# Kernel optimization log

Measured on AMD Instinct MI355X. Metric: run time of the kernel, lower is better.

The kernel has to match this reference:

```python
import jax, jax.numpy as jnp
import numpy as np

WS, SHIFT, NH, DIM = 8, 4, 4, 128
HD = DIM // NH
B, H, W = 16, 128, 128
N = WS * WS
LOG100 = float(np.log(100.0))


def _rel_tables():
    r = np.arange(-(WS - 1), WS, dtype=np.float32)
    tab = np.stack(np.meshgrid(r, r, indexing='ij'), axis=-1) / (WS - 1) * 8.0
    tab = np.sign(tab) * np.log2(np.abs(tab) + 1.0) / np.log2(8.0)
    coords = np.stack(np.meshgrid(np.arange(WS), np.arange(WS), indexing='ij')).reshape(2, -1)
    rel = (coords[:, :, None] - coords[:, None, :]).transpose(1, 2, 0).copy()
    rel[:, :, 0] += WS - 1
    rel[:, :, 1] += WS - 1
    rel[:, :, 0] *= 2 * WS - 1
    return jnp.asarray(tab.reshape(-1, 2)), jnp.asarray(rel.sum(-1))

REL_TABLE, REL_INDEX = _rel_tables()  # ((2WS-1)^2, 2), (N, N)


def _attn_mask():
    img = np.zeros((H, W), np.float32)
    cnt = 0
    for hs in (slice(0, -WS), slice(-WS, -SHIFT), slice(-SHIFT, None)):
        for ws in (slice(0, -WS), slice(-WS, -SHIFT), slice(-SHIFT, None)):
            img[hs, ws] = cnt
            cnt += 1
    mw = img.reshape(H // WS, WS, W // WS, WS).transpose(0, 2, 1, 3).reshape(-1, N)
    d = mw[:, None, :] - mw[:, :, None]
    return jnp.asarray(np.where(d != 0, -100.0, 0.0).astype(np.float32))

ATTN_MASK = _attn_mask()  # (nW, N, N)


def _ln(x, w, b, eps=1e-5):
    mu = x.mean(-1, keepdims=True)
    var = ((x - mu) ** 2).mean(-1, keepdims=True)
    return (x - mu) * jax.lax.rsqrt(var + eps) * w + b


def setup_inputs() -> dict:
    key = jax.random.key(0)
    ks = jax.random.split(key, 8)
    s = 0.02
    return {
        'x': jax.random.normal(ks[0], (B, DIM, H, W), jnp.float32),
        'norm1_w': jnp.ones((DIM,), jnp.float32),
        'norm1_b': jnp.zeros((DIM,), jnp.float32),
        'qkv_w': jax.random.normal(ks[1], (3 * DIM, DIM), jnp.float32) * s,
        'q_bias': jnp.zeros((DIM,), jnp.float32),
        'v_bias': jnp.zeros((DIM,), jnp.float32),
        'logit_scale': jnp.full((NH, 1, 1), float(np.log(10.0)), jnp.float32),
        'cpb_w1': jax.random.normal(ks[2], (512, 2), jnp.float32) * s,
        'cpb_b1': jnp.zeros((512,), jnp.float32),
        'cpb_w2': jax.random.normal(ks[3], (NH, 512), jnp.float32) * s,
        'proj_w': jax.random.normal(ks[4], (DIM, DIM), jnp.float32) * s,
        'proj_b': jnp.zeros((DIM,), jnp.float32),
        'norm2_w': jnp.ones((DIM,), jnp.float32),
        'norm2_b': jnp.zeros((DIM,), jnp.float32),
        'fc1_w': jax.random.normal(ks[5], (4 * DIM, DIM), jnp.float32) * s,
        'fc1_b': jnp.zeros((4 * DIM,), jnp.float32),
        'fc2_w': jax.random.normal(ks[6], (DIM, 4 * DIM), jnp.float32) * s,
        'fc2_b': jnp.zeros((DIM,), jnp.float32),
    }


def reference(x, norm1_w, norm1_b, qkv_w, q_bias, v_bias, logit_scale,
              cpb_w1, cpb_b1, cpb_w2, proj_w, proj_b,
              norm2_w, norm2_b, fc1_w, fc1_b, fc2_w, fc2_b):
    xb = jnp.transpose(x, (0, 2, 3, 1))                 # (B,H,W,C)
    shortcut = xb.reshape(B, H * W, DIM)
    shifted = jnp.roll(xb, (-SHIFT, -SHIFT), axis=(1, 2))
    # window partition -> (B*nW, N, C)
    xw = shifted.reshape(B, H // WS, WS, W // WS, WS, DIM)
    xw = xw.transpose(0, 1, 3, 2, 4, 5).reshape(-1, N, DIM)
    B_ = xw.shape[0]
    qkv_bias = jnp.concatenate([q_bias, jnp.zeros_like(v_bias), v_bias])
    qkv = xw @ qkv_w.T + qkv_bias
    qkv = qkv.reshape(B_, N, 3, NH, HD).transpose(2, 0, 3, 1, 4)
    q, k, v = qkv[0], qkv[1], qkv[2]                    # (B_,NH,N,HD)
    qn = q / jnp.maximum(jnp.linalg.norm(q, axis=-1, keepdims=True), 1e-12)
    kn = k / jnp.maximum(jnp.linalg.norm(k, axis=-1, keepdims=True), 1e-12)
    attn = jnp.einsum('bhnd,bhmd->bhnm', qn, kn)
    attn = attn * jnp.exp(jnp.minimum(logit_scale, LOG100))
    # continuous relative position bias: tiny MLP over log-spaced coords + gather
    tab = jax.nn.relu(REL_TABLE @ cpb_w1.T + cpb_b1) @ cpb_w2.T    # ((2WS-1)^2, NH)
    bias = tab[REL_INDEX.reshape(-1)].reshape(N, N, NH).transpose(2, 0, 1)
    attn = attn + (16.0 * jax.nn.sigmoid(bias))[None]
    nW = ATTN_MASK.shape[0]
    attn = attn.reshape(B_ // nW, nW, NH, N, N) + ATTN_MASK[None, :, None]
    attn = jax.nn.softmax(attn.reshape(B_, NH, N, N), axis=-1)
    out = jnp.einsum('bhnm,bhmd->bhnd', attn, v).transpose(0, 2, 1, 3).reshape(B_, N, DIM)
    out = out @ proj_w.T + proj_b
    # window reverse + reverse cyclic shift
    out = out.reshape(B, H // WS, W // WS, WS, WS, DIM).transpose(0, 1, 3, 2, 4, 5).reshape(B, H, W, DIM)
    out = jnp.roll(out, (SHIFT, SHIFT), axis=(1, 2)).reshape(B, H * W, DIM)
    x1 = shortcut + _ln(out, norm1_w, norm1_b)          # Swin-v2 post-norm residual
    hdn = jax.nn.silu(x1 @ fc1_w.T + fc1_b) @ fc2_w.T + fc2_b
    x2 = x1 + _ln(hdn, norm2_w, norm2_b)
    return x2.reshape(B, H, W, DIM).transpose(0, 3, 1, 2)
```

## Files before the change

### kernel.cpp

```cpp
#include <hip/hip_runtime.h>
#include <cstdint>
#include <cstddef>

typedef __bf16 bf16;
typedef __bf16 bf16x4 __attribute__((ext_vector_type(4)));
typedef __bf16 bf16x8 __attribute__((ext_vector_type(8)));
typedef float f32x4 __attribute__((ext_vector_type(4)));

#define MFMA16(a, b, c) __builtin_amdgcn_mfma_f32_16x16x32_bf16((a), (b), (c), 0, 0, 0)

__device__ __forceinline__ float bf2f(bf16 v) { return (float)v; }

__device__ __forceinline__ void pack4(float a0, float a1, float a2, float a3, bf16* dst) {
    bf16x4 v; v[0] = (bf16)a0; v[1] = (bf16)a1; v[2] = (bf16)a2; v[3] = (bf16)a3;
    *(bf16x4*)dst = v;
}

#define OFF_SCALES 65536
#define OFF_FLAG   65552
#define OFF_QKVB   65600
#define OFF_PROJB  67136
#define OFF_N1W    67648
#define OFF_N1B    68160
#define OFF_FC1B   68672
#define OFF_FC2B   70720
#define OFF_N2W    71232
#define OFF_N2B    71744
#define OFF_QKVW   73728
#define OFF_PROJW  172032
#define OFF_FC1W   204800
#define OFF_FC2W   335872

template<int DT>
__device__ __forceinline__ void g_ld4(const void* base, size_t idx, float* o) {
    if constexpr (DT == 0) {
        uint2 d = *(const uint2*)((const bf16*)base + idx);
        const bf16* p = (const bf16*)&d;
        o[0] = bf2f(p[0]); o[1] = bf2f(p[1]); o[2] = bf2f(p[2]); o[3] = bf2f(p[3]);
    } else {
        float4 d = *(const float4*)((const float*)base + idx);
        o[0] = d.x; o[1] = d.y; o[2] = d.z; o[3] = d.w;
    }
}

__global__ void k_init(const void* __restrict__ cpb_w1, const void* __restrict__ cpb_b1,
                       const void* __restrict__ cpb_w2, const void* __restrict__ logit_scale,
                       const void* __restrict__ qkv_w, const void* __restrict__ proj_w,
                       const void* __restrict__ fc1w, const void* __restrict__ fc2w,
                       const void* __restrict__ q_bias, const void* __restrict__ v_bias,
                       const void* __restrict__ proj_b, const void* __restrict__ n1w, const void* __restrict__ n1b,
                       const void* __restrict__ fc1b, const void* __restrict__ fc2b,
                       const void* __restrict__ n2w, const void* __restrict__ n2b,
                       char* __restrict__ ws)
{
    const int t = threadIdx.x;
    __shared__ int s_cnt;
    if (t == 0) s_cnt = 0;
    __syncthreads();
    {
        const unsigned short* u = (const unsigned short*)qkv_w;
        int c = 0;
        for (int i = t; i < 1024; i += 256) {
            const int e = (u[i] >> 7) & 0xFF;
            if (e >= 0x90 || (e != 0 && e <= 0x60)) ++c;
        }
        atomicAdd(&s_cnt, c);
    }
    __syncthreads();
    const int isf = (s_cnt > 64) ? 1 : 0;

    if (blockIdx.x == 0) {
        float* biasAll = (float*)ws;
        float* scales  = (float*)(ws + OFF_SCALES);
        int*   flag    = (int*)(ws + OFF_FLAG);
        if (t == 0) *flag = isf;
        __shared__ float w1s[1024];
        __shared__ float b1s[512];
        __shared__ float w2s[2048];
        __shared__ float tabv[225][4];
        if (isf) {
            const float* w1 = (const float*)cpb_w1;
            const float* b1 = (const float*)cpb_b1;
            const float* w2 = (const float*)cpb_w2;
            for (int i = t; i < 1024; i += 256) w1s[i] = w1[i];
            for (int i = t; i < 512;  i += 256) b1s[i] = b1[i];
            for (int i = t; i < 2048; i += 256) w2s[i] = w2[i];
            if (t < 4) scales[t] = expf(fminf(((const float*)logit_scale)[t], 4.6051701859880914f));
        } else {
            const bf16* w1 = (const bf16*)cpb_w1;
            const bf16* b1 = (const bf16*)cpb_b1;
            const bf16* w2 = (const bf16*)cpb_w2;
            for (int i = t; i < 1024; i += 256) w1s[i] = bf2f(w1[i]);
            for (int i = t; i < 512;  i += 256) b1s[i] = bf2f(b1[i]);
            for (int i = t; i < 2048; i += 256) w2s[i] = bf2f(w2[i]);
            if (t < 4) scales[t] = expf(fminf(bf2f(((const bf16*)logit_scale)[t]), 4.6051701859880914f));
        }
        __syncthreads();
        if (t < 225) {
            const int i = t / 15, j = t % 15;
            auto relf = [](int tt) -> float {
                float tf = (float)tt * (8.0f / 7.0f);
                float a = log2f(fabsf(tf) + 1.0f) * (1.0f / 3.0f);
                return tt < 0 ? -a : a;
            };
            const float x0 = relf(i - 7), x1 = relf(j - 7);
            float a0 = 0.f, a1 = 0.f, a2 = 0.f, a3 = 0.f;
            for (int jj = 0; jj < 512; ++jj) {
                float hv = w1s[jj*2] * x0 + w1s[jj*2+1] * x1 + b1s[jj];
                hv = fmaxf(hv, 0.0f);
                a0 += w2s[jj]        * hv;
                a1 += w2s[512 + jj]  * hv;
                a2 += w2s[1024 + jj] * hv;
                a3 += w2s[1536 + jj] * hv;
            }
            tabv[t][0] = a0; tabv[t][1] = a1; tabv[t][2] = a2; tabv[t][3] = a3;
        }
        __syncthreads();
        for (int idx = t; idx < 4*64*64; idx += 256) {
            const int h = idx >> 12, rem = idx & 4095, i = rem >> 6, j = rem & 63;
            const int di = (i >> 3) - (j >> 3) + 7;
            const int dj = (i & 7) - (j & 7) + 7;
            const float bv = tabv[di*15 + dj][h];
            biasAll[idx] = 16.0f / (1.0f + expf(-bv));
        }
    } else {
        const int g  = (blockIdx.x - 1) * 256 + t;
        const int gs = 96 * 256;
        bf16* qw = (bf16*)(ws + OFF_QKVW);
        bf16* pw = (bf16*)(ws + OFF_PROJW);
        bf16* f1 = (bf16*)(ws + OFF_FC1W);
        bf16* f2 = (bf16*)(ws + OFF_FC2W);
        if (isf) {
            const float* a = (const float*)qkv_w;  for (int i = g; i < 49152; i += gs) qw[i] = (bf16)a[i];
            const float* b = (const float*)proj_w; for (int i = g; i < 16384; i += gs) pw[i] = (bf16)b[i];
            const float* c = (const float*)fc1w;   for (int i = g; i < 65536; i += gs) f1[i] = (bf16)c[i];
            const float* d = (const float*)fc2w;   for (int i = g; i < 65536; i += gs) f2[i] = (bf16)d[i];
        } else {
            const bf16* a = (const bf16*)qkv_w;  for (int i = g; i < 49152; i += gs) qw[i] = a[i];
            const bf16* b = (const bf16*)proj_w; for (int i = g; i < 16384; i += gs) pw[i] = b[i];
            const bf16* c = (const bf16*)fc1w;   for (int i = g; i < 65536; i += gs) f1[i] = c[i];
            const bf16* d = (const bf16*)fc2w;   for (int i = g; i < 65536; i += gs) f2[i] = d[i];
        }
        auto ldf = [&](const void* p, int i) -> float {
            return isf ? ((const float*)p)[i] : bf2f(((const bf16*)p)[i]);
        };
        float* qb  = (float*)(ws + OFF_QKVB);
        float* pb  = (float*)(ws + OFF_PROJB);
        float* w1  = (float*)(ws + OFF_N1W);
        float* b1  = (float*)(ws + OFF_N1B);
        float* f1b = (float*)(ws + OFF_FC1B);
        float* f2b = (float*)(ws + OFF_FC2B);
        float* w2  = (float*)(ws + OFF_N2W);
        float* b2  = (float*)(ws + OFF_N2B);
        for (int i = g; i < 384; i += gs)
            qb[i] = (i < 128) ? ldf(q_bias, i) : ((i < 256) ? 0.0f : ldf(v_bias, i - 256));
        for (int i = g; i < 512; i += gs) f1b[i] = ldf(fc1b, i);
        for (int i = g; i < 128; i += gs) {
            pb[i]  = ldf(proj_b, i); w1[i] = ldf(n1w, i); b1[i] = ldf(n1b, i);
            f2b[i] = ldf(fc2b, i);   w2[i] = ldf(n2w, i); b2[i] = ldf(n2b, i);
        }
    }
}

__global__ __launch_bounds__(256, 3) void k_fused(
    const void* __restrict__ x,
    const bf16* __restrict__ qkvw, const float* __restrict__ qkvb,
    const bf16* __restrict__ projw, const float* __restrict__ projb,
    const float* __restrict__ n1wf, const float* __restrict__ n1bf,
    const bf16* __restrict__ fc1w, const float* __restrict__ fc1bf,
    const bf16* __restrict__ fc2w, const float* __restrict__ fc2bf,
    const float* __restrict__ n2wf, const float* __restrict__ n2bf,
    const float* __restrict__ biasAll, const float* __restrict__ scales,
    const int* __restrict__ flag, void* __restrict__ out)
{
    const int isf = *flag;

    __shared__ __align__(16) char smem[52480];
    char* XK   = smem;
    bf16* x1s  = (bf16*)smem;
    char* R3   = smem + 32768;
    bf16* Xs   = (bf16*)R3;
    bf16* Os   = (bf16*)R3;
    bf16* hs   = (bf16*)R3;
    float* psum  = (float*)(smem + 50176);
    float* invks = psum;
    float* pvar  = (float*)(smem + 51200);
    int*   rid   = (int*)(smem + 52224);

    const int tid  = threadIdx.x;
    const int wv   = tid >> 6;
    const int lane = tid & 63;
    const int l15  = lane & 15;
    const int quad = lane >> 4;

    const int bid0 = blockIdx.x;
    const int bid  = ((bid0 & 7) << 9) | (bid0 >> 3);
    const int b   = bid >> 8;
    const int wh  = (bid >> 4) & 15;
    const int ww  = bid & 15;

    {
        const int c  = tid & 127;
        const int rb = tid >> 7;
        const int w0 = ww*8 + 4;
        const int w1 = (ww*8 + 8) & 127;
#pragma unroll
        for (int k = 0; k < 4; ++k) {
            const int r    = k*2 + rb;
            const int srch = (wh*8 + r + 4) & 127;
            const size_t rowbase = (((size_t)(b*128 + c))*128 + srch)*128;
            float va[4], vb[4];
            if (isf) { g_ld4<1>(x, rowbase + w0, va); g_ld4<1>(x, rowbase + w1, vb); }
            else     { g_ld4<0>(x, rowbase + w0, va); g_ld4<0>(x, rowbase + w1, vb); }
#pragma unroll
            for (int j = 0; j < 4; ++j) {
                Xs[(r*8 + j)*136 + c]     = (bf16)va[j];
                Xs[(r*8 + 4 + j)*136 + c] = (bf16)vb[j];
            }
        }
        if (tid < 64) {
            const int rr = tid >> 3, cc = tid & 7;
            const int hs_ = wh*8 + rr, wsc = ww*8 + cc;
            const int rh = (hs_ < 120) ? 0 : ((hs_ < 124) ? 1 : 2);
            const int rw = (wsc < 120) ? 0 : ((wsc < 124) ? 1 : 2);
            rid[tid] = rh*3 + rw;
        }
    }
    __syncthreads();

    float iq[4];
    {
        f32x4 acc[6][4];
#pragma unroll
        for (int t = 0; t < 6; ++t)
#pragma unroll
            for (int mt = 0; mt < 4; ++mt) acc[t][mt] = (f32x4){0.f, 0.f, 0.f, 0.f};
#pragma unroll
        for (int ks = 0; ks < 4; ++ks) {
            bf16x8 a[4];
#pragma unroll
            for (int mt = 0; mt < 4; ++mt)
                a[mt] = *(const bf16x8*)&Xs[(mt*16 + l15)*136 + ks*32 + quad*8];
#pragma unroll
            for (int t = 0; t < 6; ++t) {
                const int wrow = (t >> 1)*128 + wv*32 + (t & 1)*16 + l15;
                bf16x8 bw = *(const bf16x8*)&qkvw[(size_t)wrow*128 + ks*32 + quad*8];
                if (t < 4) {
#pragma unroll
                    for (int mt = 0; mt < 4; ++mt)
                        acc[t][mt] = MFMA16(bw, a[mt], acc[t][mt]);
                } else {
#pragma unroll
                    for (int mt = 0; mt < 4; ++mt)
                        acc[t][mt] = MFMA16(a[mt], bw, acc[t][mt]);
                }
            }
        }
        __syncthreads();

        float sq[4] = {0.f,0.f,0.f,0.f};
        float sk[4] = {0.f,0.f,0.f,0.f};
#pragma unroll
        for (int t = 0; t < 4; ++t) {
            const int colb = (t >> 1)*128 + wv*32 + (t & 1)*16 + quad*4;
            const float4 b4 = *(const float4*)&qkvb[colb];
#pragma unroll
            for (int mt = 0; mt < 4; ++mt) {
                const int row = mt*16 + l15;
                const float v0 = acc[t][mt][0] + b4.x;
                const float v1 = acc[t][mt][1] + b4.y;
                const float v2 = acc[t][mt][2] + b4.z;
                const float v3 = acc[t][mt][3] + b4.w;
                const float ss = v0*v0 + v1*v1 + v2*v2 + v3*v3;
                if (t < 2) sq[mt] += ss; else sk[mt] += ss;
                pack4(v0, v1, v2, v3,
                      (bf16*)(XK + row*512 + ((colb*2) ^ ((row & 7) << 4))));
            }
        }
#pragma unroll
        for (int t = 4; t < 6; ++t) {
            const int vrow = wv*32 + (t & 1)*16 + l15;
            const float bb = qkvb[256 + vrow];
            char* vbase = R3 + vrow*128;
            const int rx = (vrow & 7) << 4;
#pragma unroll
            for (int mt = 0; mt < 4; ++mt) {
                const int tokb = mt*16 + quad*4;
                pack4(acc[t][mt][0] + bb, acc[t][mt][1] + bb,
                      acc[t][mt][2] + bb, acc[t][mt][3] + bb,
                      (bf16*)(vbase + ((tokb*2) ^ rx)));
            }
        }
#pragma unroll
        for (int mt = 0; mt < 4; ++mt) {
            float s2 = sq[mt];
            s2 += __shfl_xor(s2, 16); s2 += __shfl_xor(s2, 32);
            iq[mt] = 1.0f / fmaxf(sqrtf(s2), 1e-12f);
            float k2 = sk[mt];
            k2 += __shfl_xor(k2, 16); k2 += __shfl_xor(k2, 32);
            if (quad == 0) invks[wv*64 + mt*16 + l15] = 1.0f / fmaxf(sqrtf(k2), 1e-12f);
        }
    }

    {
        const float scale = scales[wv];
        f32x4 s[4][4];
#pragma unroll
        for (int jt = 0; jt < 4; ++jt)
#pragma unroll
            for (int it = 0; it < 4; ++it) s[jt][it] = (f32x4){0.f, 0.f, 0.f, 0.f};
        bf16x8 aq[4];
#pragma unroll
        for (int it = 0; it < 4; ++it) {
            const int row = it*16 + l15;
            aq[it] = *(const bf16x8*)(XK + row*512 + (((wv*32 + quad*8)*2) ^ ((row & 7) << 4)));
        }
#pragma unroll
        for (int jt = 0; jt < 4; ++jt) {
            const int row = jt*16 + l15;
            bf16x8 bk = *(const bf16x8*)(XK + row*512 + (((128 + wv*32 + quad*8)*2) ^ ((row & 7) << 4)));
#pragma unroll
            for (int it = 0; it < 4; ++it)
                s[jt][it] = MFMA16(bk, aq[it], s[jt][it]);
        }
        __syncthreads();

        const float* bg = biasAll + wv*4096;
        const bool bnd = (wh == 15) || (ww == 15);
        float iqs[4]; int ri[4];
#pragma unroll
        for (int it = 0; it < 4; ++it) {
            iqs[it] = iq[it] * scale;
            ri[it]  = rid[it*16 + l15];
        }
        float4 ikj[4]; int4 rj4[4];
#pragma unroll
        for (int jt = 0; jt < 4; ++jt) {
            ikj[jt] = *(const float4*)&invks[wv*64 + jt*16 + quad*4];
            rj4[jt] = *(const int4*)&rid[jt*16 + quad*4];
        }
#pragma unroll
        for (int it = 0; it < 4; ++it) {
            const int i = it*16 + l15;
#pragma unroll
            for (int jt = 0; jt < 4; ++jt) {
                const float4 bb = *(const float4*)&bg[i*64 + jt*16 + quad*4];
#pragma unroll
                for (int r = 0; r < 4; ++r) {
                    float v = s[jt][it][r] * (iqs[it] * ((const float*)&ikj[jt])[r]) + ((const float*)&bb)[r];
                    if (bnd && (ri[it] != ((const int*)&rj4[jt])[r])) v -= 100.0f;
                    s[jt][it][r] = v;
                }
            }
            float m = s[0][it][0];
#pragma unroll
            for (int jt = 0; jt < 4; ++jt)
#pragma unroll
                for (int r = 0; r < 4; ++r) m = fmaxf(m, s[jt][it][r]);
            m = fmaxf(m, __shfl_xor(m, 16));
            m = fmaxf(m, __shfl_xor(m, 32));
            float sm = 0.f;
#pragma unroll
            for (int jt = 0; jt < 4; ++jt)
#pragma unroll
                for (int r = 0; r < 4; ++r) {
                    const float e = __expf(s[jt][it][r] - m);
                    s[jt][it][r] = e;
                    sm += e;
                }
            sm += __shfl_xor(sm, 16);
            sm += __shfl_xor(sm, 32);
            const float inv = 1.0f / sm;
#pragma unroll
            for (int jt = 0; jt < 4; ++jt)
                pack4(s[jt][it][0]*inv, s[jt][it][1]*inv, s[jt][it][2]*inv, s[jt][it][3]*inv,
                      (bf16*)(XK + wv*8192 + i*128 + ((jt*32 + quad*8) ^ ((i & 7) << 4))));
        }
    }

    {
        f32x4 o[2][4];
#pragma unroll
        for (int dt = 0; dt < 2; ++dt)
#pragma unroll
            for (int it = 0; it < 4; ++it) o[dt][it] = (f32x4){0.f, 0.f, 0.f, 0.f};
#pragma unroll
        for (int ks = 0; ks < 2; ++ks) {
            bf16x8 bp[4];
#pragma unroll
            for (int it = 0; it < 4; ++it) {
                const int row = it*16 + l15;
                bp[it] = *(const bf16x8*)(XK + wv*8192 + row*128 + ((ks*64 + quad*16) ^ ((row & 7) << 4)));
            }
#pragma unroll
            for (int dt = 0; dt < 2; ++dt) {
                const int vrow = wv*32 + dt*16 + l15;
                bf16x8 av = *(const bf16x8*)(R3 + vrow*128 + ((ks*64 + quad*16) ^ ((vrow & 7) << 4)));
#pragma unroll
                for (int it = 0; it < 4; ++it)
                    o[dt][it] = MFMA16(av, bp[it], o[dt][it]);
            }
        }
        __syncthreads();
#pragma unroll
        for (int dt = 0; dt < 2; ++dt)
#pragma unroll
            for (int it = 0; it < 4; ++it)
                pack4(o[dt][it][0], o[dt][it][1], o[dt][it][2], o[dt][it][3],
                      &Os[(it*16 + l15)*136 + wv*32 + dt*16 + quad*4]);
    }
    __syncthreads();

    {
        float res[2][4][4];
#pragma unroll
        for (int tt = 0; tt < 4; ++tt) {
            const int tok = tt*16 + l15;
            const int hh  = (wh*8 + (tok >> 3) + 4) & 127;
            const int wwp = (ww*8 + (tok & 7) + 4) & 127;
            const size_t tb = (size_t)b*2097152 + (size_t)hh*128 + wwp;
#pragma unroll
            for (int ct = 0; ct < 2; ++ct)
#pragma unroll
                for (int r = 0; r < 4; ++r) {
                    const int c = wv*32 + ct*16 + quad*4 + r;
                    float xv;
                    if (isf) xv = ((const float*)x)[tb + (size_t)c*16384];
                    else     xv = bf2f(((const bf16*)x)[tb + (size_t)c*16384]);
                    res[ct][tt][r] = bf2f((bf16)xv);
                }
        }
        f32x4 pa[2][4];
#pragma unroll
        for (int ct = 0; ct < 2; ++ct)
#pragma unroll
            for (int tt = 0; tt < 4; ++tt) pa[ct][tt] = (f32x4){0.f, 0.f, 0.f, 0.f};
#pragma unroll
        for (int ks = 0; ks < 4; ++ks) {
            bf16x8 bo[4];
#pragma unroll
            for (int tt = 0; tt < 4; ++tt)
                bo[tt] = *(const bf16x8*)&Os[(tt*16 + l15)*136 + ks*32 + quad*8];
#pragma unroll
            for (int ct = 0; ct < 2; ++ct) {
                bf16x8 aw = *(const bf16x8*)&projw[(size_t)(wv*32 + ct*16 + l15)*128 + ks*32 + quad*8];
#pragma unroll
                for (int tt = 0; tt < 4; ++tt)
                    pa[ct][tt] = MFMA16(aw, bo[tt], pa[ct][tt]);
            }
        }
        float4 pb4[2], wn4[2], bn4[2];
#pragma unroll
        for (int ct = 0; ct < 2; ++ct) {
            const int ob = wv*32 + ct*16 + quad*4;
            pb4[ct] = *(const float4*)&projb[ob];
            wn4[ct] = *(const float4*)&n1wf[ob];
            bn4[ct] = *(const float4*)&n1bf[ob];
        }
#pragma unroll
        for (int tt = 0; tt < 4; ++tt) {
            float sv = 0.f;
#pragma unroll
            for (int ct = 0; ct < 2; ++ct)
#pragma unroll
                for (int r = 0; r < 4; ++r) {
                    pa[ct][tt][r] += ((const float*)&pb4[ct])[r];
                    sv += pa[ct][tt][r];
                }
            sv += __shfl_xor(sv, 16);
            sv += __shfl_xor(sv, 32);
            if (quad == 0) psum[wv*64 + tt*16 + l15] = sv;
        }
        __syncthreads();
        float mu[4];
#pragma unroll
        for (int tt = 0; tt < 4; ++tt) {
            const int tok = tt*16 + l15;
            mu[tt] = (psum[tok] + psum[64+tok] + psum[128+tok] + psum[192+tok]) * (1.0f/128.0f);
            float sv = 0.f;
#pragma unroll
            for (int ct = 0; ct < 2; ++ct)
#pragma unroll
                for (int r = 0; r < 4; ++r) {
                    const float d = pa[ct][tt][r] - mu[tt];
                    sv += d*d;
                }
            sv += __shfl_xor(sv, 16);
            sv += __shfl_xor(sv, 32);
            if (quad == 0) pvar[wv*64 + tok] = sv;
        }
        __syncthreads();
#pragma unroll
        for (int tt = 0; tt < 4; ++tt) {
            const int tok = tt*16 + l15;
            const float var = (pvar[tok] + pvar[64+tok] + pvar[128+tok] + pvar[192+tok]) * (1.0f/128.0f);
            const float rstd = rsqrtf(var + 1e-5f);
#pragma unroll
            for (int ct = 0; ct < 2; ++ct) {
                const int ob = wv*32 + ct*16 + quad*4;
                float xv[4];
#pragma unroll
                for (int r = 0; r < 4; ++r)
                    xv[r] = res[ct][tt][r] + (pa[ct][tt][r] - mu[tt]) * rstd * ((const float*)&wn4[ct])[r]
                            + ((const float*)&bn4[ct])[r];
                pack4(xv[0], xv[1], xv[2], xv[3], &x1s[tok*136 + ob]);
            }
        }
    }
    __syncthreads();

    f32x4 ya[2][4];
#pragma unroll
    for (int ct = 0; ct < 2; ++ct)
#pragma unroll
        for (int tt = 0; tt < 4; ++tt) ya[ct][tt] = (f32x4){0.f, 0.f, 0.f, 0.f};

#pragma unroll
    for (int ch = 0; ch < 4; ++ch) {
        if (ch) __syncthreads();
        f32x4 ha[2][4];
#pragma unroll
        for (int ht = 0; ht < 2; ++ht)
#pragma unroll
            for (int tt = 0; tt < 4; ++tt) ha[ht][tt] = (f32x4){0.f, 0.f, 0.f, 0.f};
#pragma unroll
        for (int ks = 0; ks < 4; ++ks) {
            bf16x8 bx[4];
#pragma unroll
            for (int tt = 0; tt < 4; ++tt)
                bx[tt] = *(const bf16x8*)&x1s[(tt*16 + l15)*136 + ks*32 + quad*8];
#pragma unroll
            for (int ht = 0; ht < 2; ++ht) {
                bf16x8 aw = *(const bf16x8*)&fc1w[(size_t)(ch*128 + wv*32 + ht*16 + l15)*128 + ks*32 + quad*8];
#pragma unroll
                for (int tt = 0; tt < 4; ++tt)
                    ha[ht][tt] = MFMA16(aw, bx[tt], ha[ht][tt]);
            }
        }
#pragma unroll
        for (int ht = 0; ht < 2; ++ht) {
            const float4 bb4 = *(const float4*)&fc1bf[ch*128 + wv*32 + ht*16 + quad*4];
            const int hb = wv*32 + ht*16 + quad*4;
#pragma unroll
            for (int tt = 0; tt < 4; ++tt) {
                float hv[4];
#pragma unroll
                for (int r = 0; r < 4; ++r) {
                    float v = ha[ht][tt][r] + ((const float*)&bb4)[r];
                    hv[r] = v / (1.0f + __expf(-v));
                }
                pack4(hv[0], hv[1], hv[2], hv[3], &hs[(tt*16 + l15)*136 + hb]);
            }
        }
        __syncthreads();
#pragma unroll
        for (int ks = 0; ks < 4; ++ks) {
            bf16x8 bh[4];
#pragma unroll
            for (int tt = 0; tt < 4; ++tt)
                bh[tt] = *(const bf16x8*)&hs[(tt*16 + l15)*136 + ks*32 + quad*8];
#pragma unroll
            for (int ct = 0; ct < 2; ++ct) {
                bf16x8 aw = *(const bf16x8*)&fc2w[(size_t)(wv*32 + ct*16 + l15)*512 + ch*128 + ks*32 + quad*8];
#pragma unroll
                for (int tt = 0; tt < 4; ++tt)
                    ya[ct][tt] = MFMA16(aw, bh[tt], ya[ct][tt]);
            }
        }
    }
    __syncthreads();

    {
        float4 pb4[2], wn4[2], bn4[2];
#pragma unroll
        for (int ct = 0; ct < 2; ++ct) {
            const int ob = wv*32 + ct*16 + quad*4;
            pb4[ct] = *(const float4*)&fc2bf[ob];
            wn4[ct] = *(const float4*)&n2wf[ob];
            bn4[ct] = *(const float4*)&n2bf[ob];
        }
#pragma unroll
        for (int tt = 0; tt < 4; ++tt) {
            float sv = 0.f;
#pragma unroll
            for (int ct = 0; ct < 2; ++ct)
#pragma unroll
                for (int r = 0; r < 4; ++r) {
                    ya[ct][tt][r] += ((const float*)&pb4[ct])[r];
                    sv += ya[ct][tt][r];
                }
            sv += __shfl_xor(sv, 16);
            sv += __shfl_xor(sv, 32);
            if (quad == 0) psum[wv*64 + tt*16 + l15] = sv;
        }
        __syncthreads();
        float mu[4];
#pragma unroll
        for (int tt = 0; tt < 4; ++tt) {
            const int tok = tt*16 + l15;
            mu[tt] = (psum[tok] + psum[64+tok] + psum[128+tok] + psum[192+tok]) * (1.0f/128.0f);
            float sv = 0.f;
#pragma unroll
            for (int ct = 0; ct < 2; ++ct)
#pragma unroll
                for (int r = 0; r < 4; ++r) {
                    const float d = ya[ct][tt][r] - mu[tt];
                    sv += d*d;
                }
            sv += __shfl_xor(sv, 16);
            sv += __shfl_xor(sv, 32);
            if (quad == 0) pvar[wv*64 + tok] = sv;
        }
        __syncthreads();
        bf16* x2s = hs;
#pragma unroll
        for (int tt = 0; tt < 4; ++tt) {
            const int tok = tt*16 + l15;
            const float var = (pvar[tok] + pvar[64+tok] + pvar[128+tok] + pvar[192+tok]) * (1.0f/128.0f);
            const float rstd = rsqrtf(var + 1e-5f);
#pragma unroll
            for (int ct = 0; ct < 2; ++ct) {
                const int ob = wv*32 + ct*16 + quad*4;
                bf16x4 xr = *(const bf16x4*)&x1s[tok*136 + ob];
                float xv[4];
#pragma unroll
                for (int r = 0; r < 4; ++r)
                    xv[r] = bf2f(xr[r]) + (ya[ct][tt][r] - mu[tt]) * rstd * ((const float*)&wn4[ct])[r]
                            + ((const float*)&bn4[ct])[r];
                pack4(xv[0], xv[1], xv[2], xv[3], &x2s[tok*136 + ob]);
            }
        }
    }
    __syncthreads();

    {
        const bf16* x2s = hs;
        const int wf0 = ww*8 + 4;
        const int wf1 = (ww*8 + 8) & 127;
#pragma unroll
        for (int g = 0; g < 4; ++g) {
            const int idx = g*256 + tid;
            const int c  = idx & 127;
            const int rr = idx >> 7;
            const int hf = (wh*8 + rr + 4) & 127;
            const size_t rowb = ((size_t)(b*128 + c))*16384 + (size_t)hf*128;
            if (!isf) {
                const unsigned short* xu = (const unsigned short*)x2s;
                uint2 u0, u1;
                u0.x = (unsigned)xu[(rr*8+0)*136 + c] | ((unsigned)xu[(rr*8+1)*136 + c] << 16);
                u0.y = (unsigned)xu[(rr*8+2)*136 + c] | ((unsigned)xu[(rr*8+3)*136 + c] << 16);
                u1.x = (unsigned)xu[(rr*8+4)*136 + c] | ((unsigned)xu[(rr*8+5)*136 + c] << 16);
                u1.y = (unsigned)xu[(rr*8+6)*136 + c] | ((unsigned)xu[(rr*8+7)*136 + c] << 16);
                bf16* dstb = (bf16*)out;
                *(uint2*)(dstb + rowb + wf0) = u0;
                *(uint2*)(dstb + rowb + wf1) = u1;
            } else {
                float4 u0, u1;
                u0.x = bf2f(x2s[(rr*8+0)*136 + c]); u0.y = bf2f(x2s[(rr*8+1)*136 + c]);
                u0.z = bf2f(x2s[(rr*8+2)*136 + c]); u0.w = bf2f(x2s[(rr*8+3)*136 + c]);
                u1.x = bf2f(x2s[(rr*8+4)*136 + c]); u1.y = bf2f(x2s[(rr*8+5)*136 + c]);
                u1.z = bf2f(x2s[(rr*8+6)*136 + c]); u1.w = bf2f(x2s[(rr*8+7)*136 + c]);
                float* dstf = (float*)out;
                *(float4*)(dstf + rowb + wf0) = u0;
                *(float4*)(dstf + rowb + wf1) = u1;
            }
        }
    }
}

extern "C" void kernel_launch(void* const* d_in, const int* in_sizes, int n_in,
                              void* d_out, int out_size, void* d_ws, size_t ws_size,
                              hipStream_t stream)
{
    (void)in_sizes; (void)n_in; (void)out_size; (void)ws_size;
    const void* x      = d_in[0];
    const void* n1w    = d_in[1];
    const void* n1b    = d_in[2];
    const void* qkv_w  = d_in[3];
    const void* q_bias = d_in[4];
    const void* v_bias = d_in[5];
    const void* lscale = d_in[6];
    const void* cpb_w1 = d_in[7];
    const void* cpb_b1 = d_in[8];
    const void* cpb_w2 = d_in[9];
    const void* proj_w = d_in[10];
    const void* proj_b = d_in[11];
    const void* n2w    = d_in[12];
    const void* n2b    = d_in[13];
    const void* fc1w   = d_in[14];
    const void* fc1b   = d_in[15];
    const void* fc2w   = d_in[16];
    const void* fc2b   = d_in[17];

    char*  ws      = (char*)d_ws;
    float* biasAll = (float*)ws;
    float* scales  = (float*)(ws + OFF_SCALES);
    int*   flag    = (int*)(ws + OFF_FLAG);

    k_init<<<dim3(97), dim3(256), 0, stream>>>(cpb_w1, cpb_b1, cpb_w2, lscale,
                                               qkv_w, proj_w, fc1w, fc2w,
                                               q_bias, v_bias, proj_b, n1w, n1b,
                                               fc1b, fc2b, n2w, n2b, ws);
    k_fused<<<dim3(4096), dim3(256), 0, stream>>>(x,
        (const bf16*)(ws + OFF_QKVW), (const float*)(ws + OFF_QKVB),
        (const bf16*)(ws + OFF_PROJW), (const float*)(ws + OFF_PROJB),
        (const float*)(ws + OFF_N1W), (const float*)(ws + OFF_N1B),
        (const bf16*)(ws + OFF_FC1W), (const float*)(ws + OFF_FC1B),
        (const bf16*)(ws + OFF_FC2W), (const float*)(ws + OFF_FC2B),
        (const float*)(ws + OFF_N2W), (const float*)(ws + OFF_N2B),
        biasAll, scales, flag, d_out);
}
```

Baseline: 620.8 us.

## Keep input tile resident in LDS for residual; drop aliasing and a barrier

The shared-memory layout is reorganised so the loaded input tile (Xs) stays resident for the whole kernel, with separate padded buffers for QK, V and probabilities instead of XOR-swizzled aliased regions. The residual add now reads the input tile from LDS instead of re-gathering it from global memory with strided channel loads, and one barrier after the QKV GEMM is removed because the buffers no longer overlap. LDS usage grows from about 51 KB to about 73 KB per block and the occupancy hint drops from 3 to 2 blocks per CU. This trades latency hiding for fewer global loads and barriers. Padding replaces swizzling, which may change LDS bank-conflict behaviour.

```diff
diff --git a/kernel.cpp b/kernel.cpp
--- a/kernel.cpp
+++ b/kernel.cpp
@@ -162,7 +162,7 @@
     }
 }
 
-__global__ __launch_bounds__(256, 3) void k_fused(
+__global__ __launch_bounds__(256, 2) void k_fused(
     const void* __restrict__ x,
     const bf16* __restrict__ qkvw, const float* __restrict__ qkvb,
     const bf16* __restrict__ projw, const float* __restrict__ projb,
@@ -175,17 +175,18 @@
 {
     const int isf = *flag;
 
-    __shared__ __align__(16) char smem[52480];
-    char* XK   = smem;
-    bf16* x1s  = (bf16*)smem;
-    char* R3   = smem + 32768;
-    bf16* Xs   = (bf16*)R3;
-    bf16* Os   = (bf16*)R3;
-    bf16* hs   = (bf16*)R3;
-    float* psum  = (float*)(smem + 50176);
-    float* invks = psum;
-    float* pvar  = (float*)(smem + 51200);
-    int*   rid   = (int*)(smem + 52224);
+    __shared__ __align__(16) char smem[75008];
+    bf16* Xs    = (bf16*)smem;
+    bf16* qkvs  = (bf16*)(smem + 17408);
+    bf16* PsT   = qkvs;
+    bf16* x1s   = qkvs;
+    bf16* vs    = (bf16*)(smem + 54272);
+    bf16* Os    = vs;
+    bf16* hs    = vs;
+    float* psum  = (float*)(smem + 72704);
+    float* invks = (float*)(smem + 73728);
+    float* pvar  = invks;
+    int*   rid   = (int*)(smem + 74752);
 
     const int tid  = threadIdx.x;
     const int wv   = tid >> 6;
@@ -256,8 +257,6 @@
                 }
             }
         }
-        __syncthreads();
-
         float sq[4] = {0.f,0.f,0.f,0.f};
         float sk[4] = {0.f,0.f,0.f,0.f};
 #pragma unroll
@@ -273,23 +272,18 @@
                 const float v3 = acc[t][mt][3] + b4.w;
                 const float ss = v0*v0 + v1*v1 + v2*v2 + v3*v3;
                 if (t < 2) sq[mt] += ss; else sk[mt] += ss;
-                pack4(v0, v1, v2, v3,
-                      (bf16*)(XK + row*512 + ((colb*2) ^ ((row & 7) << 4))));
+                pack4(v0, v1, v2, v3, &qkvs[row*264 + colb]);
             }
         }
 #pragma unroll
         for (int t = 4; t < 6; ++t) {
             const int vrow = wv*32 + (t & 1)*16 + l15;
             const float bb = qkvb[256 + vrow];
-            char* vbase = R3 + vrow*128;
-            const int rx = (vrow & 7) << 4;
-#pragma unroll
-            for (int mt = 0; mt < 4; ++mt) {
-                const int tokb = mt*16 + quad*4;
+#pragma unroll
+            for (int mt = 0; mt < 4; ++mt)
                 pack4(acc[t][mt][0] + bb, acc[t][mt][1] + bb,
                       acc[t][mt][2] + bb, acc[t][mt][3] + bb,
-                      (bf16*)(vbase + ((tokb*2) ^ rx)));
-            }
+                      &vs[vrow*72 + mt*16 + quad*4]);
         }
 #pragma unroll
         for (int mt = 0; mt < 4; ++mt) {
@@ -311,14 +305,11 @@
             for (int it = 0; it < 4; ++it) s[jt][it] = (f32x4){0.f, 0.f, 0.f, 0.f};
         bf16x8 aq[4];
 #pragma unroll
-        for (int it = 0; it < 4; ++it) {
-            const int row = it*16 + l15;
-            aq[it] = *(const bf16x8*)(XK + row*512 + (((wv*32 + quad*8)*2) ^ ((row & 7) << 4)));
-        }
+        for (int it = 0; it < 4; ++it)
+            aq[it] = *(const bf16x8*)&qkvs[(it*16 + l15)*264 + wv*32 + quad*8];
 #pragma unroll
         for (int jt = 0; jt < 4; ++jt) {
-            const int row = jt*16 + l15;
-            bf16x8 bk = *(const bf16x8*)(XK + row*512 + (((128 + wv*32 + quad*8)*2) ^ ((row & 7) << 4)));
+            bf16x8 bk = *(const bf16x8*)&qkvs[(jt*16 + l15)*264 + 128 + wv*32 + quad*8];
 #pragma unroll
             for (int it = 0; it < 4; ++it)
                 s[jt][it] = MFMA16(bk, aq[it], s[jt][it]);
@@ -374,7 +365,7 @@
 #pragma unroll
             for (int jt = 0; jt < 4; ++jt)
                 pack4(s[jt][it][0]*inv, s[jt][it][1]*inv, s[jt][it][2]*inv, s[jt][it][3]*inv,
-                      (bf16*)(XK + wv*8192 + i*128 + ((jt*32 + quad*8) ^ ((i & 7) << 4))));
+                      &PsT[wv*4608 + i*72 + jt*16 + quad*4]);
         }
     }
 
@@ -388,14 +379,11 @@
         for (int ks = 0; ks < 2; ++ks) {
             bf16x8 bp[4];
 #pragma unroll
-            for (int it = 0; it < 4; ++it) {
-                const int row = it*16 + l15;
-                bp[it] = *(const bf16x8*)(XK + wv*8192 + row*128 + ((ks*64 + quad*16) ^ ((row & 7) << 4)));
-            }
+            for (int it = 0; it < 4; ++it)
+                bp[it] = *(const bf16x8*)&PsT[wv*4608 + (it*16 + l15)*72 + ks*32 + quad*8];
 #pragma unroll
             for (int dt = 0; dt < 2; ++dt) {
-                const int vrow = wv*32 + dt*16 + l15;
-                bf16x8 av = *(const bf16x8*)(R3 + vrow*128 + ((ks*64 + quad*16) ^ ((vrow & 7) << 4)));
+                bf16x8 av = *(const bf16x8*)&vs[(wv*32 + dt*16 + l15)*72 + ks*32 + quad*8];
 #pragma unroll
                 for (int it = 0; it < 4; ++it)
                     o[dt][it] = MFMA16(av, bp[it], o[dt][it]);
@@ -412,24 +400,6 @@
     __syncthreads();
 
     {
-        float res[2][4][4];
-#pragma unroll
-        for (int tt = 0; tt < 4; ++tt) {
-            const int tok = tt*16 + l15;
-            const int hh  = (wh*8 + (tok >> 3) + 4) & 127;
-            const int wwp = (ww*8 + (tok & 7) + 4) & 127;
-            const size_t tb = (size_t)b*2097152 + (size_t)hh*128 + wwp;
-#pragma unroll
-            for (int ct = 0; ct < 2; ++ct)
-#pragma unroll
-                for (int r = 0; r < 4; ++r) {
-                    const int c = wv*32 + ct*16 + quad*4 + r;
-                    float xv;
-                    if (isf) xv = ((const float*)x)[tb + (size_t)c*16384];
-                    else     xv = bf2f(((const bf16*)x)[tb + (size_t)c*16384]);
-                    res[ct][tt][r] = bf2f((bf16)xv);
-                }
-        }
         f32x4 pa[2][4];
 #pragma unroll
         for (int ct = 0; ct < 2; ++ct)
@@ -498,10 +468,11 @@
 #pragma unroll
             for (int ct = 0; ct < 2; ++ct) {
                 const int ob = wv*32 + ct*16 + quad*4;
+                bf16x4 xr = *(const bf16x4*)&Xs[tok*136 + ob];
                 float xv[4];
 #pragma unroll
                 for (int r = 0; r < 4; ++r)
-                    xv[r] = res[ct][tt][r] + (pa[ct][tt][r] - mu[tt]) * rstd * ((const float*)&wn4[ct])[r]
+                    xv[r] = bf2f(xr[r]) + (pa[ct][tt][r] - mu[tt]) * rstd * ((const float*)&wn4[ct])[r]
                             + ((const float*)&bn4[ct])[r];
                 pack4(xv[0], xv[1], xv[2], xv[3], &x1s[tok*136 + ob]);
             }
```

Measured after the change: 591.0 us. 1.05x faster.

## Swizzle LDS tiles, split V projection, keep residual in registers

Applied to the files above, without the earlier changes.

Replaces the padded 136-stride shared-memory tiles with XOR-swizzled 256-byte rows and shrinks the LDS footprint. The QKV projection is split so V is computed and stored first, which lowers peak accumulator registers. The residual for the first post-norm is read from the staged input tile in LDS instead of being re-gathered from global memory with strided scalar loads. The risk is extra address arithmetic and a second pass over the A-operand loads.

```diff
diff --git a/kernel.cpp b/kernel.cpp
--- a/kernel.cpp
+++ b/kernel.cpp
@@ -8,6 +8,8 @@
 typedef float f32x4 __attribute__((ext_vector_type(4)));
 
 #define MFMA16(a, b, c) __builtin_amdgcn_mfma_f32_16x16x32_bf16((a), (b), (c), 0, 0, 0)
+
+#define SWZ(row, byteoff) ((byteoff) ^ (((row) & 7) << 4))
 
 __device__ __forceinline__ float bf2f(bf16 v) { return (float)v; }
 
@@ -175,17 +177,13 @@
 {
     const int isf = *flag;
 
-    __shared__ __align__(16) char smem[52480];
-    char* XK   = smem;
-    bf16* x1s  = (bf16*)smem;
-    char* R3   = smem + 32768;
-    bf16* Xs   = (bf16*)R3;
-    bf16* Os   = (bf16*)R3;
-    bf16* hs   = (bf16*)R3;
-    float* psum  = (float*)(smem + 50176);
-    float* invks = psum;
-    float* pvar  = (float*)(smem + 51200);
-    int*   rid   = (int*)(smem + 52224);
+    __shared__ __align__(16) char smem[51456];
+    char* A  = smem;
+    char* Bv = smem + 32768;
+    float* psum  = (float*)(smem + 49152);
+    float* invks = (float*)(smem + 50176);
+    float* pvar  = invks;
+    int*   rid   = (int*)(smem + 51200);
 
     const int tid  = threadIdx.x;
     const int wv   = tid >> 6;
@@ -214,8 +212,9 @@
             else     { g_ld4<0>(x, rowbase + w0, va); g_ld4<0>(x, rowbase + w1, vb); }
 #pragma unroll
             for (int j = 0; j < 4; ++j) {
-                Xs[(r*8 + j)*136 + c]     = (bf16)va[j];
-                Xs[(r*8 + 4 + j)*136 + c] = (bf16)vb[j];
+                const int r0 = r*8 + j, r1 = r*8 + 4 + j;
+                *(bf16*)(A + r0*256 + SWZ(r0, c*2)) = (bf16)va[j];
+                *(bf16*)(A + r1*256 + SWZ(r1, c*2)) = (bf16)vb[j];
             }
         }
         if (tid < 64) {
@@ -229,31 +228,72 @@
     __syncthreads();
 
     float iq[4];
+    bf16x4 resv[2][4];
     {
-        f32x4 acc[6][4];
-#pragma unroll
-        for (int t = 0; t < 6; ++t)
-#pragma unroll
-            for (int mt = 0; mt < 4; ++mt) acc[t][mt] = (f32x4){0.f, 0.f, 0.f, 0.f};
+        f32x4 accv[2][4];
+#pragma unroll
+        for (int t = 0; t < 2; ++t)
+#pragma unroll
+            for (int mt = 0; mt < 4; ++mt) accv[t][mt] = (f32x4){0.f, 0.f, 0.f, 0.f};
 #pragma unroll
         for (int ks = 0; ks < 4; ++ks) {
             bf16x8 a[4];
 #pragma unroll
-            for (int mt = 0; mt < 4; ++mt)
-                a[mt] = *(const bf16x8*)&Xs[(mt*16 + l15)*136 + ks*32 + quad*8];
-#pragma unroll
-            for (int t = 0; t < 6; ++t) {
+            for (int mt = 0; mt < 4; ++mt) {
+                const int row = mt*16 + l15;
+                a[mt] = *(const bf16x8*)(A + row*256 + SWZ(row, ks*64 + quad*16));
+            }
+#pragma unroll
+            for (int t = 0; t < 2; ++t) {
+                const int wrow = 256 + wv*32 + t*16 + l15;
+                bf16x8 bw = *(const bf16x8*)&qkvw[(size_t)wrow*128 + ks*32 + quad*8];
+#pragma unroll
+                for (int mt = 0; mt < 4; ++mt)
+                    accv[t][mt] = MFMA16(a[mt], bw, accv[t][mt]);
+            }
+        }
+#pragma unroll
+        for (int t = 0; t < 2; ++t) {
+            const int vrow = wv*32 + t*16 + l15;
+            const float bb = qkvb[256 + vrow];
+#pragma unroll
+            for (int mt = 0; mt < 4; ++mt) {
+                const int tokb = mt*16 + quad*4;
+                pack4(accv[t][mt][0] + bb, accv[t][mt][1] + bb,
+                      accv[t][mt][2] + bb, accv[t][mt][3] + bb,
+                      (bf16*)(Bv + vrow*128 + SWZ(vrow, tokb*2)));
+            }
+        }
+
+        f32x4 acc[4][4];
+#pragma unroll
+        for (int t = 0; t < 4; ++t)
+#pragma unroll
+            for (int mt = 0; mt < 4; ++mt) acc[t][mt] = (f32x4){0.f, 0.f, 0.f, 0.f};
+#pragma unroll
+        for (int ks = 0; ks < 4; ++ks) {
+            bf16x8 a[4];
+#pragma unroll
+            for (int mt = 0; mt < 4; ++mt) {
+                const int row = mt*16 + l15;
+                a[mt] = *(const bf16x8*)(A + row*256 + SWZ(row, ks*64 + quad*16));
+            }
+#pragma unroll
+            for (int t = 0; t < 4; ++t) {
                 const int wrow = (t >> 1)*128 + wv*32 + (t & 1)*16 + l15;
                 bf16x8 bw = *(const bf16x8*)&qkvw[(size_t)wrow*128 + ks*32 + quad*8];
-                if (t < 4) {
-#pragma unroll
-                    for (int mt = 0; mt < 4; ++mt)
-                        acc[t][mt] = MFMA16(bw, a[mt], acc[t][mt]);
-                } else {
-#pragma unroll
-                    for (int mt = 0; mt < 4; ++mt)
-                        acc[t][mt] = MFMA16(a[mt], bw, acc[t][mt]);
-                }
+#pragma unroll
+                for (int mt = 0; mt < 4; ++mt)
+                    acc[t][mt] = MFMA16(bw, a[mt], acc[t][mt]);
+            }
+        }
+#pragma unroll
+        for (int tt = 0; tt < 4; ++tt) {
+            const int tok = tt*16 + l15;
+#pragma unroll
+            for (int ct = 0; ct < 2; ++ct) {
+                const int ob = wv*32 + ct*16 + quad*4;
+                resv[ct][tt] = *(const bf16x4*)(A + tok*256 + SWZ(tok, ob*2));
             }
         }
         __syncthreads();
@@ -273,22 +313,7 @@
                 const float v3 = acc[t][mt][3] + b4.w;
                 const float ss = v0*v0 + v1*v1 + v2*v2 + v3*v3;
                 if (t < 2) sq[mt] += ss; else sk[mt] += ss;
-                pack4(v0, v1, v2, v3,
-                      (bf16*)(XK + row*512 + ((colb*2) ^ ((row & 7) << 4))));
-            }
-        }
-#pragma unroll
-        for (int t = 4; t < 6; ++t) {
-            const int vrow = wv*32 + (t & 1)*16 + l15;
-            const float bb = qkvb[256 + vrow];
-            char* vbase = R3 + vrow*128;
-            const int rx = (vrow & 7) << 4;
-#pragma unroll
-            for (int mt = 0; mt < 4; ++mt) {
-                const int tokb = mt*16 + quad*4;
-                pack4(acc[t][mt][0] + bb, acc[t][mt][1] + bb,
-                      acc[t][mt][2] + bb, acc[t][mt][3] + bb,
-                      (bf16*)(vbase + ((tokb*2) ^ rx)));
+                pack4(v0, v1, v2, v3, (bf16*)(A + row*512 + SWZ(row, colb*2)));
             }
         }
 #pragma unroll
@@ -313,12 +338,12 @@
 #pragma unroll
         for (int it = 0; it < 4; ++it) {
             const int row = it*16 + l15;
-            aq[it] = *(const bf16x8*)(XK + row*512 + (((wv*32 + quad*8)*2) ^ ((row & 7) << 4)));
+            aq[it] = *(const bf16x8*)(A + row*512 + SWZ(row, (wv*32 + quad*8)*2));
         }
 #pragma unroll
         for (int jt = 0; jt < 4; ++jt) {
             const int row = jt*16 + l15;
-            bf16x8 bk = *(const bf16x8*)(XK + row*512 + (((128 + wv*32 + quad*8)*2) ^ ((row & 7) << 4)));
+            bf16x8 bk = *(const bf16x8*)(A + row*512 + SWZ(row, (128 + wv*32 + quad*8)*2));
 #pragma unroll
             for (int it = 0; it < 4; ++it)
                 s[jt][it] = MFMA16(bk, aq[it], s[jt][it]);
@@ -374,7 +399,7 @@
 #pragma unroll
             for (int jt = 0; jt < 4; ++jt)
                 pack4(s[jt][it][0]*inv, s[jt][it][1]*inv, s[jt][it][2]*inv, s[jt][it][3]*inv,
-                      (bf16*)(XK + wv*8192 + i*128 + ((jt*32 + quad*8) ^ ((i & 7) << 4))));
+                      (bf16*)(A + wv*8192 + i*128 + SWZ(i, jt*32 + quad*8)));
         }
     }
 
@@ -390,12 +415,12 @@
 #pragma unroll
             for (int it = 0; it < 4; ++it) {
                 const int row = it*16 + l15;
-                bp[it] = *(const bf16x8*)(XK + wv*8192 + row*128 + ((ks*64 + quad*16) ^ ((row & 7) << 4)));
+                bp[it] = *(const bf16x8*)(A + wv*8192 + row*128 + SWZ(row, ks*64 + quad*16));
             }
 #pragma unroll
             for (int dt = 0; dt < 2; ++dt) {
                 const int vrow = wv*32 + dt*16 + l15;
-                bf16x8 av = *(const bf16x8*)(R3 + vrow*128 + ((ks*64 + quad*16) ^ ((vrow & 7) << 4)));
+                bf16x8 av = *(const bf16x8*)(Bv + vrow*128 + SWZ(vrow, ks*64 + quad*16));
 #pragma unroll
                 for (int it = 0; it < 4; ++it)
                     o[dt][it] = MFMA16(av, bp[it], o[dt][it]);
@@ -405,31 +430,15 @@
 #pragma unroll
         for (int dt = 0; dt < 2; ++dt)
 #pragma unroll
-            for (int it = 0; it < 4; ++it)
+            for (int it = 0; it < 4; ++it) {
+                const int tok = it*16 + l15;
                 pack4(o[dt][it][0], o[dt][it][1], o[dt][it][2], o[dt][it][3],
-                      &Os[(it*16 + l15)*136 + wv*32 + dt*16 + quad*4]);
+                      (bf16*)(Bv + tok*256 + SWZ(tok, (wv*32 + dt*16 + quad*4)*2)));
+            }
     }
     __syncthreads();
 
     {
-        float res[2][4][4];
-#pragma unroll
-        for (int tt = 0; tt < 4; ++tt) {
-            const int tok = tt*16 + l15;
-            const int hh  = (wh*8 + (tok >> 3) + 4) & 127;
-            const int wwp = (ww*8 + (tok & 7) + 4) & 127;
-            const size_t tb = (size_t)b*2097152 + (size_t)hh*128 + wwp;
-#pragma unroll
-            for (int ct = 0; ct < 2; ++ct)
-#pragma unroll
-                for (int r = 0; r < 4; ++r) {
-                    const int c = wv*32 + ct*16 + quad*4 + r;
-                    float xv;
-                    if (isf) xv = ((const float*)x)[tb + (size_t)c*16384];
-                    else     xv = bf2f(((const bf16*)x)[tb + (size_t)c*16384]);
-                    res[ct][tt][r] = bf2f((bf16)xv);
-                }
-        }
         f32x4 pa[2][4];
 #pragma unroll
         for (int ct = 0; ct < 2; ++ct)
@@ -439,8 +448,10 @@
         for (int ks = 0; ks < 4; ++ks) {
             bf16x8 bo[4];
 #pragma unroll
-            for (int tt = 0; tt < 4; ++tt)
-                bo[tt] = *(const bf16x8*)&Os[(tt*16 + l15)*136 + ks*32 + quad*8];
+            for (int tt = 0; tt < 4; ++tt) {
+                const int tok = tt*16 + l15;
+                bo[tt] = *(const bf16x8*)(Bv + tok*256 + SWZ(tok, ks*64 + quad*16));
+            }
 #pragma unroll
             for (int ct = 0; ct < 2; ++ct) {
                 bf16x8 aw = *(const bf16x8*)&projw[(size_t)(wv*32 + ct*16 + l15)*128 + ks*32 + quad*8];
@@ -501,9 +512,9 @@
                 float xv[4];
 #pragma unroll
                 for (int r = 0; r < 4; ++r)
-                    xv[r] = res[ct][tt][r] + (pa[ct][tt][r] - mu[tt]) * rstd * ((const float*)&wn4[ct])[r]
+                    xv[r] = bf2f(resv[ct][tt][r]) + (pa[ct][tt][r] - mu[tt]) * rstd * ((const float*)&wn4[ct])[r]
                             + ((const float*)&bn4[ct])[r];
-                pack4(xv[0], xv[1], xv[2], xv[3], &x1s[tok*136 + ob]);
+                pack4(xv[0], xv[1], xv[2], xv[3], (bf16*)(A + tok*256 + SWZ(tok, ob*2)));
             }
         }
     }
@@ -527,8 +538,10 @@
         for (int ks = 0; ks < 4; ++ks) {
             bf16x8 bx[4];
 #pragma unroll
-            for (int tt = 0; tt < 4; ++tt)
-                bx[tt] = *(const bf16x8*)&x1s[(tt*16 + l15)*136 + ks*32 + quad*8];
+            for (int tt = 0; tt < 4; ++tt) {
+                const int tok = tt*16 + l15;
+                bx[tt] = *(const bf16x8*)(A + tok*256 + SWZ(tok, ks*64 + quad*16));
+            }
 #pragma unroll
             for (int ht = 0; ht < 2; ++ht) {
                 bf16x8 aw = *(const bf16x8*)&fc1w[(size_t)(ch*128 + wv*32 + ht*16 + l15)*128 + ks*32 + quad*8];
@@ -543,13 +556,14 @@
             const int hb = wv*32 + ht*16 + quad*4;
 #pragma unroll
             for (int tt = 0; tt < 4; ++tt) {
+                const int tok = tt*16 + l15;
                 float hv[4];
 #pragma unroll
                 for (int r = 0; r < 4; ++r) {
                     float v = ha[ht][tt][r] + ((const float*)&bb4)[r];
                     hv[r] = v / (1.0f + __expf(-v));
                 }
-                pack4(hv[0], hv[1], hv[2], hv[3], &hs[(tt*16 + l15)*136 + hb]);
+                pack4(hv[0], hv[1], hv[2], hv[3], (bf16*)(Bv + tok*256 + SWZ(tok, hb*2)));
             }
         }
         __syncthreads();
@@ -557,8 +571,10 @@
         for (int ks = 0; ks < 4; ++ks) {
             bf16x8 bh[4];
 #pragma unroll
-            for (int tt = 0; tt < 4; ++tt)
-                bh[tt] = *(const bf16x8*)&hs[(tt*16 + l15)*136 + ks*32 + quad*8];
+            for (int tt = 0; tt < 4; ++tt) {
+                const int tok = tt*16 + l15;
+                bh[tt] = *(const bf16x8*)(Bv + tok*256 + SWZ(tok, ks*64 + quad*16));
+            }
 #pragma unroll
             for (int ct = 0; ct < 2; ++ct) {
                 bf16x8 aw = *(const bf16x8*)&fc2w[(size_t)(wv*32 + ct*16 + l15)*512 + ch*128 + ks*32 + quad*8];
@@ -612,7 +628,6 @@
             if (quad == 0) pvar[wv*64 + tok] = sv;
         }
         __syncthreads();
-        bf16* x2s = hs;
 #pragma unroll
         for (int tt = 0; tt < 4; ++tt) {
             const int tok = tt*16 + l15;
@@ -621,20 +636,19 @@
 #pragma unroll
             for (int ct = 0; ct < 2; ++ct) {
                 const int ob = wv*32 + ct*16 + quad*4;
-                bf16x4 xr = *(const bf16x4*)&x1s[tok*136 + ob];
+                bf16x4 xr = *(const bf16x4*)(A + tok*256 + SWZ(tok, ob*2));
                 float xv[4];
 #pragma unroll
                 for (int r = 0; r < 4; ++r)
                     xv[r] = bf2f(xr[r]) + (ya[ct][tt][r] - mu[tt]) * rstd * ((const float*)&wn4[ct])[r]
                             + ((const float*)&bn4[ct])[r];
-                pack4(xv[0], xv[1], xv[2], xv[3], &x2s[tok*136 + ob]);
+                pack4(xv[0], xv[1], xv[2], xv[3], (bf16*)(Bv + tok*256 + SWZ(tok, ob*2)));
             }
         }
     }
     __syncthreads();
 
     {
-        const bf16* x2s = hs;
         const int wf0 = ww*8 + 4;
         const int wf1 = (ww*8 + 8) & 127;
 #pragma unroll
@@ -644,22 +658,26 @@
             const int rr = idx >> 7;
             const int hf = (wh*8 + rr + 4) & 127;
             const size_t rowb = ((size_t)(b*128 + c))*16384 + (size_t)hf*128;
+            unsigned short xv[8];
+#pragma unroll
+            for (int k2 = 0; k2 < 8; ++k2) {
+                const int tb = rr*8 + k2;
+                xv[k2] = *(const unsigned short*)(Bv + tb*256 + SWZ(tb, c*2));
+            }
             if (!isf) {
-                const unsigned short* xu = (const unsigned short*)x2s;
                 uint2 u0, u1;
-                u0.x = (unsigned)xu[(rr*8+0)*136 + c] | ((unsigned)xu[(rr*8+1)*136 + c] << 16);
-                u0.y = (unsigned)xu[(rr*8+2)*136 + c] | ((unsigned)xu[(rr*8+3)*136 + c] << 16);
-                u1.x = (unsigned)xu[(rr*8+4)*136 + c] | ((unsigned)xu[(rr*8+5)*136 + c] << 16);
-                u1.y = (unsigned)xu[(rr*8+6)*136 + c] | ((unsigned)xu[(rr*8+7)*136 + c] << 16);
+                u0.x = (unsigned)xv[0] | ((unsigned)xv[1] << 16);
+                u0.y = (unsigned)xv[2] | ((unsigned)xv[3] << 16);
+                u1.x = (unsigned)xv[4] | ((unsigned)xv[5] << 16);
+                u1.y = (unsigned)xv[6] | ((unsigned)xv[7] << 16);
                 bf16* dstb = (bf16*)out;
                 *(uint2*)(dstb + rowb + wf0) = u0;
                 *(uint2*)(dstb + rowb + wf1) = u1;
             } else {
                 float4 u0, u1;
-                u0.x = bf2f(x2s[(rr*8+0)*136 + c]); u0.y = bf2f(x2s[(rr*8+1)*136 + c]);
-                u0.z = bf2f(x2s[(rr*8+2)*136 + c]); u0.w = bf2f(x2s[(rr*8+3)*136 + c]);
-                u1.x = bf2f(x2s[(rr*8+4)*136 + c]); u1.y = bf2f(x2s[(rr*8+5)*136 + c]);
-                u1.z = bf2f(x2s[(rr*8+6)*136 + c]); u1.w = bf2f(x2s[(rr*8+7)*136 + c]);
+                const bf16* xb = (const bf16*)xv;
+                u0.x = bf2f(xb[0]); u0.y = bf2f(xb[1]); u0.z = bf2f(xb[2]); u0.w = bf2f(xb[3]);
+                u1.x = bf2f(xb[4]); u1.y = bf2f(xb[5]); u1.z = bf2f(xb[6]); u1.w = bf2f(xb[7]);
                 float* dstf = (float*)out;
                 *(float4*)(dstf + rowb + wf0) = u0;
                 *(float4*)(dstf + rowb + wf1) = u1;
```

Result: faster. 578.6 us (-6.8%).
